# Kernel tuning notes

Hardware: AMD Instinct MI355X
Metric: run time of the kernel (lower is better)

## Reference

```python
import jax, jax.numpy as jnp
import numpy as np

T = 0.07      # temperature (init arg t)
K = 50        # self.k in the module
TOPK = 4096   # hardcoded top-k over the memory bank


def setup_inputs() -> dict:
    key = jax.random.key(0)
    k1, k2, k3 = jax.random.split(key, 3)
    B, N, D = 256, 262144, 256
    points = jax.random.normal(k1, (B, D), dtype=jnp.float32)
    mb = jax.random.normal(k2, (N, D), dtype=jnp.float32)
    # memory bank stores L2-normalized embeddings (NPID-style)
    memory_bank = mb / jnp.linalg.norm(mb, axis=1, keepdims=True)
    point_indices = jax.random.randint(k3, (B,), 0, N)
    return {"points": points, "memory_bank": memory_bank,
            "point_indices": point_indices, "first": 0}


def reference(points, memory_bank, point_indices, first):
    # l2_normalize(points)
    norm_points = points / jnp.linalg.norm(points, axis=1, keepdims=True)
    # memory_bank.get_all_dot_products -> [B, N], then exp(./t)
    points_sim = jnp.exp(jnp.einsum('bd,nd->bn', norm_points, memory_bank) / T)
    B = points_sim.shape[0]
    positive_sim = points_sim[jnp.arange(B), point_indices]        # [B]
    # topk(k=4096, largest=True, sorted=True)
    hn_sim, hn_idx = jax.lax.top_k(points_sim, TOPK)               # [B, 4096]
    denom = hn_sim.sum(axis=1)                                     # [B]
    loss1 = -jnp.mean(jnp.log(positive_sim / denom + 1e-07))
    if first:  # static python flag
        return loss1
    has_self = (hn_idx[:, :K + 1] == point_indices[:, None]).sum(axis=1)  # [B]
    all_other_positive_sim = hn_sim[:, :K + 1].sum(axis=1) - has_self * positive_sim
    loss2 = -jnp.mean(jnp.log(all_other_positive_sim / denom))
    return (loss1, loss2)
```

## Files before the change

### kernel.cpp

```cpp
#include <hip/hip_runtime.h>

typedef __attribute__((ext_vector_type(8))) short bf16x8;
typedef __attribute__((ext_vector_type(4))) float f32x4;

#define TINV 14.285714285714286f
#define TH0  0.10f
#define CAP  16384
#define NB   4096
#define HLO  0.10f
#define HSC  10240.0f
#define LDT  72

__device__ __forceinline__ unsigned short f2bf(float x) {
  union { float f; unsigned u; } c; c.f = x;
  return (unsigned short)((c.u + 0x7fffu + ((c.u >> 16) & 1u)) >> 16);
}

__device__ __forceinline__ int bin_of(float v) {
  int b = (int)((v - HLO) * HSC);
  b = b < 0 ? 0 : b;
  return b > (NB - 1) ? (NB - 1) : b;
}

__global__ void prep_kernel(const float* __restrict__ points,
                            const float* __restrict__ bank,
                            const int* __restrict__ pidx,
                            unsigned short* __restrict__ Abf,
                            float* __restrict__ pos_exact,
                            unsigned* __restrict__ g_cnt) {
  const int r = blockIdx.x;
  const int d = threadIdx.x;
  const int lane = d & 63, w = d >> 6;
  __shared__ float sred[4];
  __shared__ float s_norm;
  const float p = points[r * 256 + d];
  float sq = p * p;
  #pragma unroll
  for (int o = 32; o; o >>= 1) sq += __shfl_down(sq, o);
  if (lane == 0) sred[w] = sq;
  __syncthreads();
  if (d == 0) s_norm = sqrtf(sred[0] + sred[1] + sred[2] + sred[3]);
  __syncthreads();
  const float nv = p / s_norm;
  Abf[r * 256 + d] = f2bf(nv);
  float pd = nv * bank[(long)pidx[r] * 256 + d];
  __syncthreads();
  #pragma unroll
  for (int o = 32; o; o >>= 1) pd += __shfl_down(pd, o);
  if (lane == 0) sred[w] = pd;
  __syncthreads();
  if (d == 0) {
    pos_exact[r] = sred[0] + sred[1] + sred[2] + sred[3];
    g_cnt[r] = 0;
  }
}

__global__ __launch_bounds__(512) void gemm_filter(
    const unsigned short* __restrict__ Abf,
    const float* __restrict__ bank,
    const int* __restrict__ pidx,
    float* __restrict__ buf,
    unsigned* __restrict__ g_cnt,
    float* __restrict__ posv) {
  __shared__ __align__(16) char smem[(256 * LDT + 128 * LDT) * 2];
  __shared__ int s_pidx[256];
  unsigned short* lA = (unsigned short*)smem;
  unsigned short* lB = (unsigned short*)(smem + 256 * LDT * 2);
  const int tid = threadIdx.x;
  const long c0 = (long)blockIdx.x * 128;
  if (tid < 256) s_pidx[tid] = pidx[tid];
  const int w = tid >> 6, lane = tid & 63, quad = lane >> 4, l15 = lane & 15;
  f32x4 acc[2][8];
  #pragma unroll
  for (int i = 0; i < 2; ++i)
    #pragma unroll
    for (int j = 0; j < 8; ++j) acc[i][j] = (f32x4){0.f, 0.f, 0.f, 0.f};

  for (int kc = 0; kc < 4; ++kc) {
    const int k0 = kc * 64;
    if (kc) __syncthreads();
    #pragma unroll
    for (int it = 0; it < 4; ++it) {
      const int idx = it * 512 + tid;
      const int row = idx >> 3, seg = idx & 7;
      const uint4 v = *(const uint4*)(Abf + row * 256 + k0 + seg * 8);
      *(uint4*)(lA + row * LDT + seg * 8) = v;
    }
    #pragma unroll
    for (int it = 0; it < 4; ++it) {
      const int idx = it * 512 + tid;
      const int nn = idx >> 4, seg = idx & 15;
      const float4 f = *(const float4*)(bank + (c0 + nn) * 256 + k0 + seg * 4);
      ushort4 h;
      h.x = f2bf(f.x); h.y = f2bf(f.y); h.z = f2bf(f.z); h.w = f2bf(f.w);
      *(ushort4*)(lB + nn * LDT + seg * 4) = h;
    }
    __syncthreads();
    #pragma unroll
    for (int ks = 0; ks < 2; ++ks) {
      const int ko = ks * 32 + quad * 8;
      const bf16x8 a0 = *(const bf16x8*)(lA + (w * 32 + l15) * LDT + ko);
      const bf16x8 a1 = *(const bf16x8*)(lA + (w * 32 + 16 + l15) * LDT + ko);
      #pragma unroll
      for (int cf = 0; cf < 8; ++cf) {
        const bf16x8 b = *(const bf16x8*)(lB + (cf * 16 + l15) * LDT + ko);
        acc[0][cf] = __builtin_amdgcn_mfma_f32_16x16x32_bf16(a0, b, acc[0][cf], 0, 0, 0);
        acc[1][cf] = __builtin_amdgcn_mfma_f32_16x16x32_bf16(a1, b, acc[1][cf], 0, 0, 0);
      }
    }
  }
  __syncthreads();
  unsigned* e_cnt = (unsigned*)smem;
  float* e_buf = (float*)(smem + 1024);
  if (tid < 256) e_cnt[tid] = 0;
  __syncthreads();
  #pragma unroll
  for (int rf = 0; rf < 2; ++rf) {
    #pragma unroll
    for (int j = 0; j < 4; ++j) {
      const int row = w * 32 + rf * 16 + quad * 4 + j;
      const int prow = s_pidx[row];
      #pragma unroll
      for (int cf = 0; cf < 8; ++cf) {
        const float v = acc[rf][cf][j];
        const long col = c0 + cf * 16 + l15;
        if (col == prow) posv[row] = v;
        if (v > TH0) {
          const unsigned slot = atomicAdd(&e_cnt[row], 1u);
          if (slot < 48u) e_buf[row * 48 + slot] = v;
          else {
            const unsigned g = atomicAdd(&g_cnt[row], 1u);
            if (g < CAP) buf[(long)row * CAP + g] = v;
          }
        }
      }
    }
  }
  __syncthreads();
  if (tid < 256) {
    unsigned nn = e_cnt[tid];
    nn = nn > 48u ? 48u : nn;
    if (nn) {
      const unsigned base = atomicAdd(&g_cnt[tid], nn);
      for (unsigned i = 0; i < nn; ++i) {
        const unsigned p = base + i;
        if (p < CAP) buf[(long)tid * CAP + p] = e_buf[tid * 48 + i];
      }
    }
  }
}

__global__ void finalize_kernel(const float* __restrict__ buf,
                                const unsigned* __restrict__ g_cnt,
                                const float* __restrict__ posv,
                                const float* __restrict__ pos_exact,
                                float* __restrict__ term1,
                                float* __restrict__ term2) {
  const int r = blockIdx.x;
  const int tid = threadIdx.x;
  const int lane = tid & 63, w = tid >> 6;
  __shared__ unsigned hist[NB];
  __shared__ unsigned segsum[256];
  __shared__ float arr4[1024];
  __shared__ float arr51[128];
  __shared__ unsigned s_cnt4, s_cnt51;
  __shared__ int s_b4, s_b51;
  __shared__ unsigned s_cab4, s_cab51;
  __shared__ float rE[4], rE51[4];

  for (int i = tid; i < NB; i += 256) hist[i] = 0;
  if (tid == 0) { s_cnt4 = 0; s_cnt51 = 0; }
  __syncthreads();
  unsigned n = g_cnt[r];
  if (n > CAP) n = CAP;
  const float* rowbuf = buf + (long)r * CAP;
  for (unsigned i = tid; i < n; i += 256)
    atomicAdd(&hist[bin_of(rowbuf[i])], 1u);
  __syncthreads();
  unsigned ss = 0;
  #pragma unroll
  for (int j = 0; j < 16; ++j) ss += hist[tid * 16 + j];
  segsum[tid] = ss;
  __syncthreads();
  if (tid == 0) {
    unsigned cum = 0;
    int b4 = -1, b51 = -1; unsigned cab4 = 0, cab51 = 0;
    for (int s = 255; s >= 0; --s) {
      const unsigned sv = segsum[s];
      if (b51 < 0 && cum + sv >= 51u) {
        unsigned c = cum;
        for (int b = s * 16 + 15; b >= s * 16; --b) {
          const unsigned h = hist[b];
          if (c + h >= 51u) { b51 = b; cab51 = c; break; }
          c += h;
        }
      }
      if (b4 < 0 && cum + sv >= 4096u) {
        unsigned c = cum;
        for (int b = s * 16 + 15; b >= s * 16; --b) {
          const unsigned h = hist[b];
          if (c + h >= 4096u) { b4 = b; cab4 = c; break; }
          c += h;
        }
      }
      cum += sv;
      if (b4 >= 0) break;
    }
    if (b51 < 0) { b51 = 0; cab51 = 0; }
    if (b4 < 0) { b4 = 0; cab4 = 0; }
    s_b4 = b4; s_b51 = b51; s_cab4 = cab4; s_cab51 = cab51;
  }
  __syncthreads();
  const int b4 = s_b4, b51 = s_b51;
  float E = 0.f, E51 = 0.f;
  for (unsigned i = tid; i < n; i += 256) {
    const float v = rowbuf[i];
    const int b = bin_of(v);
    if (b > b4) {
      const float e = __expf(v * TINV);
      E += e;
      if (b > b51) E51 += e;
    }
    if (b == b4) {
      const unsigned s = atomicAdd(&s_cnt4, 1u);
      if (s < 1024u) arr4[s] = v;
    }
    if (b == b51) {
      const unsigned s = atomicAdd(&s_cnt51, 1u);
      if (s < 128u) arr51[s] = v;
    }
  }
  __syncthreads();
  int n4 = (int)s_cnt4; n4 = n4 > 1024 ? 1024 : n4;
  int m4 = 4096 - (int)s_cab4; m4 = m4 < 0 ? 0 : (m4 > n4 ? n4 : m4);
  int n51 = (int)s_cnt51; n51 = n51 > 128 ? 128 : n51;
  int m51 = 51 - (int)s_cab51; m51 = m51 < 0 ? 0 : (m51 > n51 ? n51 : m51);
  for (int t = tid; t < n4; t += 256) {
    const float v = arr4[t];
    int g = 0;
    for (int j = 0; j < n4; ++j) {
      const float u = arr4[j];
      g += (u > v) || (u == v && j < t);
    }
    if (g < m4) E += __expf(v * TINV);
  }
  for (int t = tid; t < n51; t += 256) {
    const float v = arr51[t];
    int g = 0;
    for (int j = 0; j < n51; ++j) {
      const float u = arr51[j];
      g += (u > v) || (u == v && j < t);
    }
    if (g < m51) E51 += __expf(v * TINV);
  }
  #pragma unroll
  for (int o = 32; o; o >>= 1) { E += __shfl_down(E, o); E51 += __shfl_down(E51, o); }
  if (lane == 0) { rE[w] = E; rE51[w] = E51; }
  __syncthreads();
  if (tid == 0) {
    const float denom = rE[0] + rE[1] + rE[2] + rE[3];
    const float top51 = rE51[0] + rE51[1] + rE51[2] + rE51[3];
    const float pv = posv[r];
    const int pb = bin_of(pv);
    int hs = 0;
    if (pb > b51) hs = 1;
    else if (pb == b51) {
      int g = 0;
      for (int j = 0; j < n51; ++j) g += (arr51[j] > pv);
      if (g < m51) hs = 1;
    }
    const float pe = __expf(pos_exact[r] * TINV);
    const float ao = top51 - (hs ? __expf(pv * TINV) : 0.f);
    term1[r] = logf(pe / denom + 1e-7f);
    term2[r] = logf(ao / denom);
  }
}

__global__ void reduce_loss(const float* __restrict__ term1,
                            const float* __restrict__ term2,
                            float* __restrict__ out) {
  __shared__ float r1[4], r2[4];
  const int tid = threadIdx.x, lane = tid & 63, w = tid >> 6;
  float t1 = term1[tid], t2 = term2[tid];
  #pragma unroll
  for (int o = 32; o; o >>= 1) { t1 += __shfl_down(t1, o); t2 += __shfl_down(t2, o); }
  if (lane == 0) { r1[w] = t1; r2[w] = t2; }
  __syncthreads();
  if (tid == 0) {
    out[0] = -(r1[0] + r1[1] + r1[2] + r1[3]) * (1.0f / 256.0f);
    out[1] = -(r2[0] + r2[1] + r2[2] + r2[3]) * (1.0f / 256.0f);
  }
}

extern "C" void kernel_launch(void* const* d_in, const int* in_sizes, int n_in,
                              void* d_out, int out_size, void* d_ws, size_t ws_size,
                              hipStream_t stream) {
  const float* points = (const float*)d_in[0];
  const float* bank   = (const float*)d_in[1];
  const int*   pidx   = (const int*)d_in[2];
  float* out = (float*)d_out;
  char* ws = (char*)d_ws;
  unsigned short* Abf = (unsigned short*)ws;
  float* pos_exact = (float*)(ws + 131072);
  float* posv      = (float*)(ws + 132096);
  unsigned* g_cnt  = (unsigned*)(ws + 133120);
  float* term1     = (float*)(ws + 134144);
  float* term2     = (float*)(ws + 135168);
  float* buf       = (float*)(ws + 136192);

  prep_kernel<<<256, 256, 0, stream>>>(points, bank, pidx, Abf, pos_exact, g_cnt);
  gemm_filter<<<262144 / 128, 512, 0, stream>>>(Abf, bank, pidx, buf, g_cnt, posv);
  finalize_kernel<<<256, 256, 0, stream>>>(buf, g_cnt, posv, pos_exact, term1, term2);
  reduce_loss<<<1, 256, 0, stream>>>(term1, term2, out);
}
```

Baseline: 488.4 us.

## Keep full A tile in LDS and stream bank directly into MFMA registers

The GEMM kernel now loads the whole 256x256 bf16 normalized-points matrix into LDS once per block. Each wave reads its 16 bank columns straight from global memory into registers, converting to bf16 with packed conversion when available and prefetching the next k-chunk. This removes the per-k-chunk LDS staging of the bank tile and the barriers that went with it. Blocks grow to 1024 threads covering 256 columns, and each wave holds 16 accumulators spanning all 256 rows. The cost is a larger LDS footprint per block, reloading A in every block, more register pressure, and strided per-lane global loads of the bank.

```diff
diff --git a/kernel.cpp b/kernel.cpp
--- a/kernel.cpp
+++ b/kernel.cpp
@@ -9,7 +9,7 @@
 #define NB   4096
 #define HLO  0.10f
 #define HSC  10240.0f
-#define LDT  72
+#define LDP  264
 
 __device__ __forceinline__ unsigned short f2bf(float x) {
   union { float f; unsigned u; } c; c.f = x;
@@ -55,83 +55,82 @@
   }
 }
 
-__global__ __launch_bounds__(512) void gemm_filter(
+__global__ __launch_bounds__(1024, 4) void gemm_filter(
     const unsigned short* __restrict__ Abf,
     const float* __restrict__ bank,
     const int* __restrict__ pidx,
     float* __restrict__ buf,
     unsigned* __restrict__ g_cnt,
     float* __restrict__ posv) {
-  __shared__ __align__(16) char smem[(256 * LDT + 128 * LDT) * 2];
+  __shared__ __align__(16) char smem[256 * LDP * 2];
   __shared__ int s_pidx[256];
   unsigned short* lA = (unsigned short*)smem;
-  unsigned short* lB = (unsigned short*)(smem + 256 * LDT * 2);
   const int tid = threadIdx.x;
-  const long c0 = (long)blockIdx.x * 128;
   if (tid < 256) s_pidx[tid] = pidx[tid];
+  #pragma unroll
+  for (int it = 0; it < 8; ++it) {
+    const int idx = it * 1024 + tid;
+    const int row = idx >> 5, seg = idx & 31;
+    *(uint4*)(lA + row * LDP + seg * 8) = *(const uint4*)(Abf + row * 256 + seg * 8);
+  }
+  __syncthreads();
+
   const int w = tid >> 6, lane = tid & 63, quad = lane >> 4, l15 = lane & 15;
-  f32x4 acc[2][8];
-  #pragma unroll
-  for (int i = 0; i < 2; ++i)
+  const long col = (long)blockIdx.x * 256 + w * 16 + l15;
+  const float* bp = bank + col * 256;
+  f32x4 acc[16];
+  #pragma unroll
+  for (int rb = 0; rb < 16; ++rb) acc[rb] = (f32x4){0.f, 0.f, 0.f, 0.f};
+
+  float4 pfa = *(const float4*)(bp + quad * 8);
+  float4 pfb = *(const float4*)(bp + quad * 8 + 4);
+  #pragma unroll
+  for (int kk = 0; kk < 8; ++kk) {
+    const float4 f0 = pfa, f1 = pfb;
+    if (kk < 7) {
+      pfa = *(const float4*)(bp + (kk + 1) * 32 + quad * 8);
+      pfb = *(const float4*)(bp + (kk + 1) * 32 + quad * 8 + 4);
+    }
+    bf16x8 b;
+#if __has_builtin(__builtin_amdgcn_cvt_pk_bf16_f32)
+    typedef __attribute__((ext_vector_type(2))) short bf16x2;
+    *(bf16x2*)&b[0] = __builtin_amdgcn_cvt_pk_bf16_f32(f0.x, f0.y);
+    *(bf16x2*)&b[2] = __builtin_amdgcn_cvt_pk_bf16_f32(f0.z, f0.w);
+    *(bf16x2*)&b[4] = __builtin_amdgcn_cvt_pk_bf16_f32(f1.x, f1.y);
+    *(bf16x2*)&b[6] = __builtin_amdgcn_cvt_pk_bf16_f32(f1.z, f1.w);
+#else
+    b[0] = (short)f2bf(f0.x); b[1] = (short)f2bf(f0.y);
+    b[2] = (short)f2bf(f0.z); b[3] = (short)f2bf(f0.w);
+    b[4] = (short)f2bf(f1.x); b[5] = (short)f2bf(f1.y);
+    b[6] = (short)f2bf(f1.z); b[7] = (short)f2bf(f1.w);
+#endif
+    const unsigned short* ab = lA + l15 * LDP + kk * 32 + quad * 8;
     #pragma unroll
-    for (int j = 0; j < 8; ++j) acc[i][j] = (f32x4){0.f, 0.f, 0.f, 0.f};
-
-  for (int kc = 0; kc < 4; ++kc) {
-    const int k0 = kc * 64;
-    if (kc) __syncthreads();
-    #pragma unroll
-    for (int it = 0; it < 4; ++it) {
-      const int idx = it * 512 + tid;
-      const int row = idx >> 3, seg = idx & 7;
-      const uint4 v = *(const uint4*)(Abf + row * 256 + k0 + seg * 8);
-      *(uint4*)(lA + row * LDT + seg * 8) = v;
-    }
-    #pragma unroll
-    for (int it = 0; it < 4; ++it) {
-      const int idx = it * 512 + tid;
-      const int nn = idx >> 4, seg = idx & 15;
-      const float4 f = *(const float4*)(bank + (c0 + nn) * 256 + k0 + seg * 4);
-      ushort4 h;
-      h.x = f2bf(f.x); h.y = f2bf(f.y); h.z = f2bf(f.z); h.w = f2bf(f.w);
-      *(ushort4*)(lB + nn * LDT + seg * 4) = h;
-    }
-    __syncthreads();
-    #pragma unroll
-    for (int ks = 0; ks < 2; ++ks) {
-      const int ko = ks * 32 + quad * 8;
-      const bf16x8 a0 = *(const bf16x8*)(lA + (w * 32 + l15) * LDT + ko);
-      const bf16x8 a1 = *(const bf16x8*)(lA + (w * 32 + 16 + l15) * LDT + ko);
-      #pragma unroll
-      for (int cf = 0; cf < 8; ++cf) {
-        const bf16x8 b = *(const bf16x8*)(lB + (cf * 16 + l15) * LDT + ko);
-        acc[0][cf] = __builtin_amdgcn_mfma_f32_16x16x32_bf16(a0, b, acc[0][cf], 0, 0, 0);
-        acc[1][cf] = __builtin_amdgcn_mfma_f32_16x16x32_bf16(a1, b, acc[1][cf], 0, 0, 0);
-      }
-    }
-  }
-  __syncthreads();
+    for (int rb = 0; rb < 16; ++rb) {
+      const bf16x8 a = *(const bf16x8*)(ab + rb * 16 * LDP);
+      acc[rb] = __builtin_amdgcn_mfma_f32_16x16x32_bf16(a, b, acc[rb], 0, 0, 0);
+    }
+  }
+  __syncthreads();
+
   unsigned* e_cnt = (unsigned*)smem;
   float* e_buf = (float*)(smem + 1024);
   if (tid < 256) e_cnt[tid] = 0;
   __syncthreads();
-  #pragma unroll
-  for (int rf = 0; rf < 2; ++rf) {
+  const int icol = (int)col;
+  #pragma unroll
+  for (int rb = 0; rb < 16; ++rb) {
     #pragma unroll
     for (int j = 0; j < 4; ++j) {
-      const int row = w * 32 + rf * 16 + quad * 4 + j;
-      const int prow = s_pidx[row];
-      #pragma unroll
-      for (int cf = 0; cf < 8; ++cf) {
-        const float v = acc[rf][cf][j];
-        const long col = c0 + cf * 16 + l15;
-        if (col == prow) posv[row] = v;
-        if (v > TH0) {
-          const unsigned slot = atomicAdd(&e_cnt[row], 1u);
-          if (slot < 48u) e_buf[row * 48 + slot] = v;
-          else {
-            const unsigned g = atomicAdd(&g_cnt[row], 1u);
-            if (g < CAP) buf[(long)row * CAP + g] = v;
-          }
+      const float v = acc[rb][j];
+      const int row = rb * 16 + quad * 4 + j;
+      if (icol == s_pidx[row]) posv[row] = v;
+      if (v > TH0) {
+        const unsigned slot = atomicAdd(&e_cnt[row], 1u);
+        if (slot < 48u) e_buf[row * 48 + slot] = v;
+        else {
+          const unsigned g = atomicAdd(&g_cnt[row], 1u);
+          if (g < CAP) buf[(long)row * CAP + g] = v;
         }
       }
     }
@@ -309,7 +308,7 @@
   float* buf       = (float*)(ws + 136192);
 
   prep_kernel<<<256, 256, 0, stream>>>(points, bank, pidx, Abf, pos_exact, g_cnt);
-  gemm_filter<<<262144 / 128, 512, 0, stream>>>(Abf, bank, pidx, buf, g_cnt, posv);
+  gemm_filter<<<262144 / 256, 1024, 0, stream>>>(Abf, bank, pidx, buf, g_cnt, posv);
   finalize_kernel<<<256, 256, 0, stream>>>(buf, g_cnt, posv, pos_exact, term1, term2);
   reduce_loss<<<1, 256, 0, stream>>>(term1, term2, out);
 }
```

New measurement: 470.3 us. 3.7% less time.

## Double-buffer GEMM via direct global-to-LDS loads with 32x32 MFMA tiles

Applied to the files above, without the earlier changes.

The GEMM-filter kernel is restructured. A and the fp32 bank tile are now streamed into double-buffered LDS with global_load_lds, so loads of the next K chunk overlap the MFMAs of the current one. The query matrix is pre-swizzled in prep into MFMA fragment order. The kernel now uses 256 threads with 32x32x16 bf16 MFMAs and 8 accumulator tiles per wave. fp32 to bf16 conversion of the bank moves to after the LDS read. The cost is doubled LDS footprint for fp32 bank data, fewer waves per block, and a smaller per-row staging buffer for threshold hits.

```diff
diff --git a/kernel.cpp b/kernel.cpp
--- a/kernel.cpp
+++ b/kernel.cpp
@@ -1,7 +1,7 @@
 #include <hip/hip_runtime.h>
 
 typedef __attribute__((ext_vector_type(8))) short bf16x8;
-typedef __attribute__((ext_vector_type(4))) float f32x4;
+typedef __attribute__((ext_vector_type(16))) float f32x16;
 
 #define TINV 14.285714285714286f
 #define TH0  0.10f
@@ -9,7 +9,7 @@
 #define NB   4096
 #define HLO  0.10f
 #define HSC  10240.0f
-#define LDT  72
+#define EPC  40
 
 __device__ __forceinline__ unsigned short f2bf(float x) {
   union { float f; unsigned u; } c; c.f = x;
@@ -22,10 +22,16 @@
   return b > (NB - 1) ? (NB - 1) : b;
 }
 
+__device__ __forceinline__ void cp16(const void* g, void* lds) {
+  __builtin_amdgcn_global_load_lds(
+      (const __attribute__((address_space(1))) unsigned*)g,
+      (__attribute__((address_space(3))) unsigned*)lds, 16, 0, 0);
+}
+
 __global__ void prep_kernel(const float* __restrict__ points,
                             const float* __restrict__ bank,
                             const int* __restrict__ pidx,
-                            unsigned short* __restrict__ Abf,
+                            unsigned short* __restrict__ Ag,
                             float* __restrict__ pos_exact,
                             unsigned* __restrict__ g_cnt) {
   const int r = blockIdx.x;
@@ -42,7 +48,11 @@
   if (d == 0) s_norm = sqrtf(sred[0] + sred[1] + sred[2] + sred[3]);
   __syncthreads();
   const float nv = p / s_norm;
-  Abf[r * 256 + d] = f2bf(nv);
+  {
+    const int t = r >> 5, fl = (((d >> 3) & 1) << 5) | (r & 31);
+    const int kg = d >> 4, j = d & 7;
+    Ag[(((t * 16 + kg) * 64 + fl) << 3) + j] = f2bf(nv);
+  }
   float pd = nv * bank[(long)pidx[r] * 256 + d];
   __syncthreads();
   #pragma unroll
@@ -55,79 +65,97 @@
   }
 }
 
-__global__ __launch_bounds__(512) void gemm_filter(
-    const unsigned short* __restrict__ Abf,
+__global__ __launch_bounds__(256, 2) void gemm_filter(
+    const unsigned short* __restrict__ Ag,
     const float* __restrict__ bank,
     const int* __restrict__ pidx,
     float* __restrict__ buf,
     unsigned* __restrict__ g_cnt,
     float* __restrict__ posv) {
-  __shared__ __align__(16) char smem[(256 * LDT + 128 * LDT) * 2];
+  __shared__ __align__(16) char smem[65536];
   __shared__ int s_pidx[256];
-  unsigned short* lA = (unsigned short*)smem;
-  unsigned short* lB = (unsigned short*)(smem + 256 * LDT * 2);
   const int tid = threadIdx.x;
+  if (tid < 256) s_pidx[tid] = pidx[tid];
+  const int w = tid >> 6, lane = tid & 63;
+  const int c32 = lane & 31, khalf = lane >> 5;
   const long c0 = (long)blockIdx.x * 128;
-  if (tid < 256) s_pidx[tid] = pidx[tid];
-  const int w = tid >> 6, lane = tid & 63, quad = lane >> 4, l15 = lane & 15;
-  f32x4 acc[2][8];
-  #pragma unroll
-  for (int i = 0; i < 2; ++i)
-    #pragma unroll
-    for (int j = 0; j < 8; ++j) acc[i][j] = (f32x4){0.f, 0.f, 0.f, 0.f};
-
-  for (int kc = 0; kc < 4; ++kc) {
-    const int k0 = kc * 64;
-    if (kc) __syncthreads();
-    #pragma unroll
-    for (int it = 0; it < 4; ++it) {
-      const int idx = it * 512 + tid;
-      const int row = idx >> 3, seg = idx & 7;
-      const uint4 v = *(const uint4*)(Abf + row * 256 + k0 + seg * 8);
-      *(uint4*)(lA + row * LDT + seg * 8) = v;
-    }
-    #pragma unroll
-    for (int it = 0; it < 4; ++it) {
-      const int idx = it * 512 + tid;
-      const int nn = idx >> 4, seg = idx & 15;
-      const float4 f = *(const float4*)(bank + (c0 + nn) * 256 + k0 + seg * 4);
-      ushort4 h;
-      h.x = f2bf(f.x); h.y = f2bf(f.y); h.z = f2bf(f.z); h.w = f2bf(f.w);
-      *(ushort4*)(lB + nn * LDT + seg * 4) = h;
+
+  f32x16 acc[8];
+  #pragma unroll
+  for (int t = 0; t < 8; ++t)
+    #pragma unroll
+    for (int r = 0; r < 16; ++r) acc[t][r] = 0.f;
+
+  auto stage = [&](int bufi, int c) {
+    char* Ab = smem + bufi * 16384;
+    char* Bb = smem + 32768 + bufi * 16384;
+    #pragma unroll
+    for (int s = 0; s < 4; ++s) {
+      const int i = w * 4 + s;
+      const int t = i >> 1, ksub = i & 1;
+      cp16(Ag + (((t * 16 + c * 2 + ksub) * 64 + lane) << 3), Ab + i * 1024);
+    }
+    #pragma unroll
+    for (int s = 0; s < 4; ++s) {
+      const int i = w * 4 + s;
+      const int kk = s >> 1, half = s & 1;
+      cp16(bank + (c0 + w * 32 + c32) * 256 + c * 32 + kk * 16 + khalf * 8 + half * 4,
+           Bb + i * 1024);
+    }
+  };
+
+  stage(0, 0);
+  __syncthreads();
+  for (int c = 0; c < 8; ++c) {
+    const int cur = c & 1;
+    if (c < 7) stage(cur ^ 1, c + 1);
+    const char* Ab = smem + cur * 16384;
+    const char* Bb = smem + 32768 + cur * 16384;
+    bf16x8 bf[4][2];
+    #pragma unroll
+    for (int tc = 0; tc < 4; ++tc)
+      #pragma unroll
+      for (int kk = 0; kk < 2; ++kk) {
+        const char* fb = Bb + (tc * 2 + kk) * 2048 + lane * 16;
+        float4 lo = *(const float4*)(fb);
+        float4 hi = *(const float4*)(fb + 1024);
+        unsigned* bu = (unsigned*)&bf[tc][kk];
+        bu[0] = (unsigned)f2bf(lo.x) | ((unsigned)f2bf(lo.y) << 16);
+        bu[1] = (unsigned)f2bf(lo.z) | ((unsigned)f2bf(lo.w) << 16);
+        bu[2] = (unsigned)f2bf(hi.x) | ((unsigned)f2bf(hi.y) << 16);
+        bu[3] = (unsigned)f2bf(hi.z) | ((unsigned)f2bf(hi.w) << 16);
+      }
+    #pragma unroll
+    for (int tr = 0; tr < 2; ++tr) {
+      #pragma unroll
+      for (int kk = 0; kk < 2; ++kk) {
+        const bf16x8 a = *(const bf16x8*)(Ab + (((w * 2 + tr) * 2 + kk) * 64 + lane) * 16);
+        #pragma unroll
+        for (int tc = 0; tc < 4; ++tc)
+          acc[tr * 4 + tc] =
+              __builtin_amdgcn_mfma_f32_32x32x16_bf16(a, bf[tc][kk], acc[tr * 4 + tc], 0, 0, 0);
+      }
     }
     __syncthreads();
-    #pragma unroll
-    for (int ks = 0; ks < 2; ++ks) {
-      const int ko = ks * 32 + quad * 8;
-      const bf16x8 a0 = *(const bf16x8*)(lA + (w * 32 + l15) * LDT + ko);
-      const bf16x8 a1 = *(const bf16x8*)(lA + (w * 32 + 16 + l15) * LDT + ko);
-      #pragma unroll
-      for (int cf = 0; cf < 8; ++cf) {
-        const bf16x8 b = *(const bf16x8*)(lB + (cf * 16 + l15) * LDT + ko);
-        acc[0][cf] = __builtin_amdgcn_mfma_f32_16x16x32_bf16(a0, b, acc[0][cf], 0, 0, 0);
-        acc[1][cf] = __builtin_amdgcn_mfma_f32_16x16x32_bf16(a1, b, acc[1][cf], 0, 0, 0);
-      }
-    }
-  }
-  __syncthreads();
+  }
+
   unsigned* e_cnt = (unsigned*)smem;
   float* e_buf = (float*)(smem + 1024);
   if (tid < 256) e_cnt[tid] = 0;
   __syncthreads();
   #pragma unroll
-  for (int rf = 0; rf < 2; ++rf) {
-    #pragma unroll
-    for (int j = 0; j < 4; ++j) {
-      const int row = w * 32 + rf * 16 + quad * 4 + j;
-      const int prow = s_pidx[row];
+  for (int tr = 0; tr < 2; ++tr) {
+    #pragma unroll
+    for (int tc = 0; tc < 4; ++tc) {
+      const int icol = (int)c0 + tc * 32 + c32;
       #pragma unroll
-      for (int cf = 0; cf < 8; ++cf) {
-        const float v = acc[rf][cf][j];
-        const long col = c0 + cf * 16 + l15;
-        if (col == prow) posv[row] = v;
+      for (int r = 0; r < 16; ++r) {
+        const float v = acc[tr * 4 + tc][r];
+        const int row = w * 64 + tr * 32 + (r & 3) + 8 * (r >> 2) + 4 * khalf;
+        if (icol == s_pidx[row]) posv[row] = v;
         if (v > TH0) {
           const unsigned slot = atomicAdd(&e_cnt[row], 1u);
-          if (slot < 48u) e_buf[row * 48 + slot] = v;
+          if (slot < EPC) e_buf[row * EPC + slot] = v;
           else {
             const unsigned g = atomicAdd(&g_cnt[row], 1u);
             if (g < CAP) buf[(long)row * CAP + g] = v;
@@ -139,12 +167,12 @@
   __syncthreads();
   if (tid < 256) {
     unsigned nn = e_cnt[tid];
-    nn = nn > 48u ? 48u : nn;
+    nn = nn > (unsigned)EPC ? (unsigned)EPC : nn;
     if (nn) {
       const unsigned base = atomicAdd(&g_cnt[tid], nn);
       for (unsigned i = 0; i < nn; ++i) {
         const unsigned p = base + i;
-        if (p < CAP) buf[(long)tid * CAP + p] = e_buf[tid * 48 + i];
+        if (p < CAP) buf[(long)tid * CAP + p] = e_buf[tid * EPC + i];
       }
     }
   }
@@ -300,7 +328,7 @@
   const int*   pidx   = (const int*)d_in[2];
   float* out = (float*)d_out;
   char* ws = (char*)d_ws;
-  unsigned short* Abf = (unsigned short*)ws;
+  unsigned short* Ag = (unsigned short*)ws;
   float* pos_exact = (float*)(ws + 131072);
   float* posv      = (float*)(ws + 132096);
   unsigned* g_cnt  = (unsigned*)(ws + 133120);
@@ -308,8 +336,8 @@
   float* term2     = (float*)(ws + 135168);
   float* buf       = (float*)(ws + 136192);
 
-  prep_kernel<<<256, 256, 0, stream>>>(points, bank, pidx, Abf, pos_exact, g_cnt);
-  gemm_filter<<<262144 / 128, 512, 0, stream>>>(Abf, bank, pidx, buf, g_cnt, posv);
+  prep_kernel<<<256, 256, 0, stream>>>(points, bank, pidx, Ag, pos_exact, g_cnt);
+  gemm_filter<<<262144 / 128, 256, 0, stream>>>(Ag, bank, pidx, buf, g_cnt, posv);
   finalize_kernel<<<256, 256, 0, stream>>>(buf, g_cnt, posv, pos_exact, term1, term2);
   reduce_loss<<<1, 256, 0, stream>>>(term1, term2, out);
 }
```

Measured after the change: 517.4 us. 5.9% more time.
